# Kernel optimization log

Measured on AMD Instinct MI355X. Metric: run time of the kernel, lower is better.

The kernel has to match this reference:

```python
import jax, jax.numpy as jnp
import numpy as np
from jax import lax


def _l2n(t, eps=1e-12):
    n = jnp.sqrt(jnp.sum(t * t, axis=-1, keepdims=True))
    return t / jnp.maximum(n, eps)


def _ln(t, w, b, eps=1e-5):
    mu = jnp.mean(t, -1, keepdims=True)
    var = jnp.var(t, -1, keepdims=True)
    return (t - mu) / jnp.sqrt(var + eps) * w + b


def _unfold3(x):
    # nn.Unfold(kernel_size=3, padding=1, stride=1): [B,C,H,W] -> [B,C,9,H*W]
    B, C, H, W = x.shape
    xp = jnp.pad(x, ((0, 0), (0, 0), (1, 1), (1, 1)))
    pat = jnp.stack([xp[:, :, i:i + H, j:j + W] for i in range(3) for j in range(3)], axis=2)
    return pat.reshape(B, C, 9, H * W)


def _forward(x, norm1_w, norm1_b, q_w, q_b, kv_w, kv_b, temperature, query_embedding,
             learnable_tokens, learnable_bias, sr_w, sr_b, pln_w, pln_b, proj_w, proj_b,
             norm2_w, norm2_b, fc1_w, fc1_b, dw_w, dw_b, fc2_w, fc2_b):
    B, C, H, W = x.shape
    nh = temperature.shape[0]
    d = C // nh
    N = H * W
    K = 9  # local_len = window_size**2
    # norm1 (WithBias LayerNorm over channel dim, channels-last)
    y = _ln(x.reshape(B, C, N).transpose(0, 2, 1), norm1_w, norm1_b)  # [B,N,C]
    # ---- AggregatedAttention ----
    q = (y @ q_w.T + q_b).reshape(B, N, nh, d).transpose(0, 2, 1, 3)  # [B,h,N,d]
    qn = _l2n(q)
    qs = (qn + query_embedding) * jax.nn.softplus(temperature)
    kv = y @ kv_w.T + kv_b  # [B,N,2C]
    k_loc = _l2n(kv[..., :C].reshape(B, N, nh, d)).reshape(B, N, C)
    kvl = jnp.concatenate([k_loc, kv[..., C:]], -1).transpose(0, 2, 1).reshape(B, 2 * C, H, W)
    pat = _unfold3(kvl).reshape(B, 2 * nh, d, K, N).transpose(0, 1, 4, 2, 3)  # [B,2h,N,d,K]
    k_l, v_l = pat[:, :nh], pat[:, nh:]
    attn_local = jnp.einsum('bhnd,bhndk->bhnk', qs, k_l)  # [B,h,N,K]
    # pooled branch; sr_ratio=1 so adaptive_avg_pool2d is identity
    y4 = y.transpose(0, 2, 1).reshape(B, C, H, W)
    xp = jax.nn.gelu(jnp.einsum('oc,bchw->bohw', sr_w, y4) + sr_b[:, None, None], approximate=False)
    xp = _ln(xp.reshape(B, C, N).transpose(0, 2, 1), pln_w, pln_b)  # [B,pool_len,C]
    kvp = (xp @ kv_w.T + kv_b).reshape(B, N, 2 * nh, d).transpose(0, 2, 1, 3)
    k_p = _l2n(kvp[:, :nh])
    v_p = kvp[:, nh:]
    attn_pool = jnp.einsum('bhnd,bhmd->bhnm', qs, k_p)  # [B,h,N,pool_len]
    attn = jax.nn.softmax(jnp.concatenate([attn_local, attn_pool], -1), axis=-1)
    a_l, a_p = attn[..., :K], attn[..., K:]
    w_l = jnp.einsum('bhnd,hdk->bhnk', qn, learnable_tokens) + learnable_bias + a_l
    x_local = jnp.einsum('bhnk,bhndk->bhnd', w_l, v_l)
    x_pool = jnp.einsum('bhnm,bhmd->bhnd', a_p, v_p)
    xo = (x_local + x_pool).transpose(0, 2, 1, 3).reshape(B, N, C)
    # proj then raw torch-style reshape [B,N,C] -> [B,C,H,W] (memory reinterpretation)
    xo = (xo @ proj_w.T + proj_b).reshape(B, C, H, W)
    x = x + xo
    # ---- ConvolutionalGLU MLP ----
    hf = dw_b.shape[0]
    y2 = _ln(x.reshape(B, C, N).transpose(0, 2, 1), norm2_w, norm2_b).transpose(0, 2, 1).reshape(B, C, H, W)
    f1 = jnp.einsum('oc,bchw->bohw', fc1_w, y2) + fc1_b[:, None, None]
    a, v = f1[:, :hf], f1[:, hf:]
    dw = lax.conv_general_dilated(a, dw_w, (1, 1), ((1, 1), (1, 1)),
                                  feature_group_count=hf,
                                  dimension_numbers=('NCHW', 'OIHW', 'NCHW')) + dw_b[:, None, None]
    g = jax.nn.gelu(dw, approximate=False) * v
    out = jnp.einsum('oc,bchw->bohw', fc2_w, g) + fc2_b[:, None, None]
    return x + out


def setup_inputs() -> dict:
    key = jax.random.key(0)
    B, C, H, W = 2, 128, 56, 56
    nh, d, K = 4, 32, 9
    hf = int(2 * int(C * 4.0) / 3)  # 341
    ks = iter(jax.random.split(key, 16))
    rn = lambda shape, s=0.02: jax.random.normal(next(ks), shape, jnp.float32) * s
    return {
        'x': jax.random.normal(next(ks), (B, C, H, W), jnp.float32),
        'norm1_w': jnp.ones((C,), jnp.float32), 'norm1_b': jnp.zeros((C,), jnp.float32),
        'q_w': rn((C, C)), 'q_b': jnp.zeros((C,), jnp.float32),
        'kv_w': rn((2 * C, C)), 'kv_b': jnp.zeros((2 * C,), jnp.float32),
        'temperature': jnp.full((nh, 1, 1), float(np.log(np.exp(1.0 / 0.24) - 1.0)), jnp.float32),
        'query_embedding': rn((nh, 1, d)),
        'learnable_tokens': rn((nh, d, K)),
        'learnable_bias': jnp.zeros((nh, 1, K), jnp.float32),
        'sr_w': rn((C, C)), 'sr_b': jnp.zeros((C,), jnp.float32),
        'pln_w': jnp.ones((C,), jnp.float32), 'pln_b': jnp.zeros((C,), jnp.float32),
        'proj_w': rn((C, C)), 'proj_b': jnp.zeros((C,), jnp.float32),
        'norm2_w': jnp.ones((C,), jnp.float32), 'norm2_b': jnp.zeros((C,), jnp.float32),
        'fc1_w': rn((2 * hf, C)), 'fc1_b': jnp.zeros((2 * hf,), jnp.float32),
        'dw_w': rn((hf, 1, 3, 3)), 'dw_b': jnp.zeros((hf,), jnp.float32),
        'fc2_w': rn((C, hf)), 'fc2_b': jnp.zeros((C,), jnp.float32),
    }


def reference(x, norm1_w, norm1_b, q_w, q_b, kv_w, kv_b, temperature, query_embedding,
              learnable_tokens, learnable_bias, sr_w, sr_b, pln_w, pln_b, proj_w, proj_b,
              norm2_w, norm2_b, fc1_w, fc1_b, dw_w, dw_b, fc2_w, fc2_b):
    return _forward(x, norm1_w, norm1_b, q_w, q_b, kv_w, kv_b, temperature, query_embedding,
                    learnable_tokens, learnable_bias, sr_w, sr_b, pln_w, pln_b, proj_w, proj_b,
                    norm2_w, norm2_b, fc1_w, fc1_b, dw_w, dw_b, fc2_w, fc2_b)
```

## Files before the change

### kernel.cpp

```cpp
#include <hip/hip_runtime.h>
#include <hip/hip_bf16.h>

typedef __hip_bfloat16 bf16;
typedef short s8v __attribute__((ext_vector_type(8)));
typedef short s4v __attribute__((ext_vector_type(4)));
typedef float f4v __attribute__((ext_vector_type(4)));

#define DEVI __device__ __forceinline__

DEVI float cvt(float x){ return x; }
DEVI float cvt(bf16 x){ return __bfloat162float(x); }

DEVI void stg(float* p, float v){ *p = v; }
DEVI void stg(bf16* p, float v){ *p = __float2bfloat16(v); }

DEVI float gelu_exact(float x){
  return 0.5f*x*(1.0f + erff(x*0.70710678118654752440f));
}

constexpr int B_ = 2, C_ = 128, H_ = 56, W_ = 56, N_ = 3136, NH_ = 4, D_ = 32, HF_ = 341;
constexpr int ROWS_ = B_*N_;
constexpr int KF2 = 352;
constexpr int GQ_ = NH_*B_*N_;
constexpr int FW = 512;
constexpr int KSP = 12;
constexpr int SPLIT = 256;
constexpr float LOG2E = 1.4426950408889634f;
constexpr float E8L2  = 11.541560327111707f;

template<typename TX, typename TY, bool PLANES>
__global__ __launch_bounds__(256)
void ln_kernel(const TX* __restrict__ x, long xstr, const float* __restrict__ w,
               const float* __restrict__ bia, TY* __restrict__ y)
{
  int gid = blockIdx.x*4 + (threadIdx.x>>6);
  int lane = threadIdx.x & 63;
  int b = gid / N_, n = gid % N_;
  float v0, v1;
  if (PLANES){
    v0 = cvt(x[((long)b*C_ + lane     )*N_ + n]);
    v1 = cvt(x[((long)b*C_ + lane + 64)*N_ + n]);
  } else {
    v0 = cvt(x[(long)gid*xstr + lane     ]);
    v1 = cvt(x[(long)gid*xstr + lane + 64]);
  }
  float s = v0+v1, ss = v0*v0 + v1*v1;
  #pragma unroll
  for (int o=32;o>0;o>>=1){ s += __shfl_xor(s,o); ss += __shfl_xor(ss,o); }
  float mu  = s*(1.0f/128.0f);
  float var = fmaxf(ss*(1.0f/128.0f) - mu*mu, 0.f);
  float inv = rsqrtf(var + 1e-5f);
  stg(&y[(long)gid*C_ + lane     ], (v0-mu)*inv*w[lane     ] + bia[lane     ]);
  stg(&y[(long)gid*C_ + lane + 64], (v1-mu)*inv*w[lane + 64] + bia[lane + 64]);
}

__global__ __launch_bounds__(256)
void head_kernel(const float* __restrict__ q_w, const float* __restrict__ kv_w,
                 const float* __restrict__ sr_w, const float* __restrict__ proj_w,
                 const float* __restrict__ fc1_w, const float* __restrict__ fc2_w,
                 const float* __restrict__ q_b, const float* __restrict__ kv_b,
                 const float* __restrict__ sr_b,
                 bf16* __restrict__ out, float* __restrict__ bias_out,
                 const float* __restrict__ x_in, const float* __restrict__ n1w,
                 const float* __restrict__ n1b, bf16* __restrict__ y)
{
  if (blockIdx.x >= 839){
    int gid = (blockIdx.x - 839)*4 + (threadIdx.x>>6);
    int lane = threadIdx.x & 63;
    int b = gid / N_, n = gid % N_;
    float v0 = x_in[((long)b*C_ + lane     )*N_ + n];
    float v1 = x_in[((long)b*C_ + lane + 64)*N_ + n];
    float s = v0+v1, ss = v0*v0 + v1*v1;
    #pragma unroll
    for (int o=32;o>0;o>>=1){ s += __shfl_xor(s,o); ss += __shfl_xor(ss,o); }
    float mu  = s*(1.0f/128.0f);
    float var = fmaxf(ss*(1.0f/128.0f) - mu*mu, 0.f);
    float inv = rsqrtf(var + 1e-5f);
    y[(long)gid*C_ + lane     ] = __float2bfloat16((v0-mu)*inv*n1w[lane     ] + n1b[lane     ]);
    y[(long)gid*C_ + lane + 64] = __float2bfloat16((v1-mu)*inv*n1w[lane + 64] + n1b[lane + 64]);
    return;
  }
  int t = blockIdx.x*256 + threadIdx.x;
  if (t >= 214272){
    int i = t - 214272;
    if (i < 512){
      float bv = (i < 128) ? q_b[i] : (i < 384) ? kv_b[i-128] : sr_b[i-384];
      bias_out[i] = bv;
    }
    return;
  }
  float v;
  if      (t <  16384) v = q_w[t];
  else if (t <  49152) v = kv_w[t-16384];
  else if (t <  65536) v = sr_w[t-49152];
  else if (t <  81920) v = proj_w[t-65536];
  else if (t < 169216) v = fc1_w[t-81920];
  else {
    int i = t - 169216; int m = i / KF2, kp = i % KF2;
    v = (kp < HF_) ? fc2_w[m*HF_ + kp] : 0.f;
  }
  out[t] = __float2bfloat16(v);
}

template<int KT, int MODE, typename TC, int BM=64, int LDA=KT, int NCH=1>
__global__ __launch_bounds__(256)
void gemm_mfma(const bf16* __restrict__ A, const bf16* __restrict__ B,
               const float* __restrict__ bias, const float* __restrict__ res,
               TC* __restrict__ Cm, int M, int Nn,
               long sA, long sB, long sC, long sR,
               const float* __restrict__ qe, const float* __restrict__ temp,
               bf16* __restrict__ aux0, bf16* __restrict__ aux1)
{
  A  += (long)blockIdx.z * sA;
  B  += (long)blockIdx.z * sB;
  Cm += (long)blockIdx.z * sC;
  if (res) res += (long)blockIdx.z * sR;
  int lane = threadIdx.x & 63, w = threadIdx.x >> 6;
  int m = lane & 15, quad = lane >> 4;
  int n0 = blockIdx.x*64, m0 = blockIdx.y*BM;
  const bf16* ap[NCH];
  #pragma unroll
  for (int cc=0; cc<NCH; cc++){
    int ar = m0 + cc*64 + w*16 + m;
    if (ar >= M) ar = M-1;
    ap[cc] = A + (long)ar*LDA + quad*8;
  }
  const bf16* bp = B + (long)(n0 + m)*KT + quad*8;
  s8v a4[KT/32];
  if (MODE==7){
    float s=0.f, ssum=0.f;
    #pragma unroll
    for (int i=0;i<KT/32;i++){
      a4[i] = *(const s8v*)(ap[0] + i*32);
      #pragma unroll
      for (int j=0;j<8;j++){
        float v = cvt(((const bf16*)&a4[i])[j]);
        s += v; ssum = fmaf(v,v,ssum);
      }
    }
    s    += __shfl_xor(s,16);    s    += __shfl_xor(s,32);
    ssum += __shfl_xor(ssum,16); ssum += __shfl_xor(ssum,32);
    float mu  = s*(1.0f/128.0f);
    float var = fmaxf(ssum*(1.0f/128.0f) - mu*mu, 0.f);
    float inv = rsqrtf(var + 1e-5f);
    #pragma unroll
    for (int i=0;i<KT/32;i++){
      #pragma unroll
      for (int j=0;j<8;j++){
        int c = i*32 + quad*8 + j;
        float v = cvt(((const bf16*)&a4[i])[j]);
        ((bf16*)&a4[i])[j] = __float2bfloat16((v-mu)*inv*qe[c] + temp[c]);
      }
    }
  }
  f4v acc[NCH][4];
  #pragma unroll
  for (int cc=0; cc<NCH; cc++)
    #pragma unroll
    for (int s=0;s<4;s++) acc[cc][s] = (f4v){0.f,0.f,0.f,0.f};
  #pragma unroll
  for (int k0 = 0; k0 < KT; k0 += 32){
    s8v bf[4];
    #pragma unroll
    for (int s=0;s<4;s++) bf[s] = *(const s8v*)(bp + (long)s*16*KT + k0);
    #pragma unroll
    for (int cc=0; cc<NCH; cc++){
      s8v af = (MODE==7) ? a4[k0/32] : *(const s8v*)(ap[cc] + k0);
      #pragma unroll
      for (int s=0;s<4;s++)
        acc[cc][s] = __builtin_amdgcn_mfma_f32_16x16x32_bf16(af, bf[s], acc[cc][s], 0, 0, 0);
    }
  }
  if ((MODE==6 || MODE==7) && blockIdx.x < 2){
    int hA = blockIdx.x*2, hB = hA+1;
    float spA = 0.f, spB = 0.f;
    if (MODE==6){
      spA = log1pf(expf(temp[hA])) * LOG2E;
      spB = log1pf(expf(temp[hB])) * LOG2E;
    }
    #pragma unroll
    for (int cc=0; cc<NCH; cc++){
      #pragma unroll
      for (int r=0;r<4;r++){
        float v4[4];
        #pragma unroll
        for (int s=0;s<4;s++) v4[s] = acc[cc][s][r] + bias[n0 + s*16 + m];
        float ssA = v4[0]*v4[0] + v4[1]*v4[1];
        float ssB = v4[2]*v4[2] + v4[3]*v4[3];
        #pragma unroll
        for (int off=1; off<16; off<<=1){
          ssA += __shfl_xor(ssA, off);
          ssB += __shfl_xor(ssB, off);
        }
        float invA = 1.f/fmaxf(sqrtf(ssA), 1e-12f);
        float invB = 1.f/fmaxf(sqrtf(ssB), 1e-12f);
        int gm = m0 + cc*64 + w*16 + quad*4 + r;
        int b = gm / N_, n = gm % N_;
        #pragma unroll
        for (int s=0;s<4;s++){
          int h = (s<2) ? hA : hB;
          int d = (s&1)*16 + m;
          float v = v4[s] * ((s<2) ? invA : invB);
          if (MODE==6) v = (v + qe[h*D_ + d]) * ((s<2) ? spA : spB);
          aux0[((long)(b*NH_+h)*N_ + n)*D_ + d] = __float2bfloat16(v);
        }
      }
    }
    return;
  }
  if (MODE==7){
    int gm0 = m0 + w*16 + quad*4;
    int b = gm0 / N_, nb = gm0 % N_;
    #pragma unroll
    for (int s=0;s<4;s++){
      int h = (blockIdx.x-2)*2 + (s>>1);
      int d = (s&1)*16 + m;
      bf16 p4[4];
      #pragma unroll
      for (int r=0;r<4;r++) p4[r] = __float2bfloat16(acc[0][s][r] + bias[n0 + s*16 + m]);
      *(s4v*)(aux1 + ((long)(b*NH_+h)*D_ + d)*N_ + nb) = *(const s4v*)p4;
    }
    return;
  }
  #pragma unroll
  for (int cc=0; cc<NCH; cc++){
    int m0c = m0 + cc*64;
    #pragma unroll
    for (int s=0;s<4;s++){
      int gn = n0 + s*16 + m;
      #pragma unroll
      for (int r=0;r<4;r++){
        int gm = m0c + w*16 + quad*4 + r;
        if (gm >= M) continue;
        float v = acc[cc][s][r];
        if (MODE==1 || MODE==4 || MODE==6) v += bias[gn];
        else                               v += bias[gm];
        if (MODE==6 && gn >= 384) v = gelu_exact(v);
        if (MODE==4 || MODE==5) v += res[(long)gm*Nn + gn];
        stg(&Cm[(long)gm*Nn + gn], v);
      }
    }
  }
}

__global__ __launch_bounds__(256)
void attn_part_kernel(const bf16* __restrict__ qs_, const bf16* __restrict__ kp_,
                      const bf16* __restrict__ vp_,
                      bf16* __restrict__ Op, float* __restrict__ Lp)
{
  int bh = blockIdx.y;
  int z  = blockIdx.z;
  int lane = threadIdx.x & 63;
  int w    = threadIdx.x >> 6;
  int m    = lane & 15, quad = lane >> 4;
  int base = blockIdx.x*256 + w*16;

  s8v af[4]; bool hasQ[4];
  #pragma unroll
  for (int ch=0; ch<4; ch++){
    int qq = base + ch*64;
    hasQ[ch] = (qq < N_);
    af[ch] = *(const s8v*)(qs_ + ((long)bh*N_ + (hasQ[ch] ? qq : base) + m)*D_ + quad*8);
  }
  const bf16* kpb = kp_ + (long)bh*N_*D_;
  const bf16* vpb = vp_ + (long)bh*D_*N_;
  int kperm = (m & 3) + 8*(m >> 2);
  f4v o0[4], o1[4];
  float l[4];
  #pragma unroll
  for (int ch=0; ch<4; ch++){
    o0[ch] = (f4v){0.f,0.f,0.f,0.f}; o1[ch] = (f4v){0.f,0.f,0.f,0.f};
    l[ch] = 0.f;
  }

  auto loadKV = [&](s8v* kf, s8v* vf, int t){
    kf[0] = *(const s8v*)(kpb + (long)(t + kperm     )*D_ + quad*8);
    kf[1] = *(const s8v*)(kpb + (long)(t + kperm +  4)*D_ + quad*8);
    kf[2] = *(const s8v*)(kpb + (long)(t + kperm + 32)*D_ + quad*8);
    kf[3] = *(const s8v*)(kpb + (long)(t + kperm + 36)*D_ + quad*8);
    vf[0] = *(const s8v*)(vpb + (long)(m     )*N_ + t      + quad*8);
    vf[1] = *(const s8v*)(vpb + (long)(16 + m)*N_ + t      + quad*8);
    vf[2] = *(const s8v*)(vpb + (long)(m     )*N_ + t + 32 + quad*8);
    vf[3] = *(const s8v*)(vpb + (long)(16 + m)*N_ + t + 32 + quad*8);
  };
  auto compute = [&](const s8v* kf, const s8v* vf){
    __builtin_amdgcn_s_setprio(1);
    #pragma unroll
    for (int ch=0; ch<4; ch++){
      f4v c[4];
      #pragma unroll
      for (int s=0;s<4;s++){
        c[s] = (f4v){-E8L2, -E8L2, -E8L2, -E8L2};
        c[s] = __builtin_amdgcn_mfma_f32_16x16x32_bf16(kf[s], af[ch], c[s], 0, 0, 0);
      }
      bf16 p8a[8], p8b[8];
      float ls = 0.f;
      #pragma unroll
      for (int r=0;r<4;r++){
        float ea = __builtin_amdgcn_exp2f(c[0][r]);
        float eb = __builtin_amdgcn_exp2f(c[1][r]);
        float ec = __builtin_amdgcn_exp2f(c[2][r]);
        float ed = __builtin_amdgcn_exp2f(c[3][r]);
        ls += (ea+eb) + (ec+ed);
        p8a[r] = __float2bfloat16(ea); p8a[4+r] = __float2bfloat16(eb);
        p8b[r] = __float2bfloat16(ec); p8b[4+r] = __float2bfloat16(ed);
      }
      l[ch] += ls;
      s8v pa = *(const s8v*)p8a, pb = *(const s8v*)p8b;
      o0[ch] = __builtin_amdgcn_mfma_f32_16x16x32_bf16(pa, vf[0], o0[ch], 0, 0, 0);
      o1[ch] = __builtin_amdgcn_mfma_f32_16x16x32_bf16(pa, vf[1], o1[ch], 0, 0, 0);
      o0[ch] = __builtin_amdgcn_mfma_f32_16x16x32_bf16(pb, vf[2], o0[ch], 0, 0, 0);
      o1[ch] = __builtin_amdgcn_mfma_f32_16x16x32_bf16(pb, vf[3], o1[ch], 0, 0, 0);
    }
    __builtin_amdgcn_s_setprio(0);
  };

  int tlo = z*SPLIT, thi = (z==KSP-1) ? N_ : tlo + SPLIT;
  s8v kfA[4], vfA[4], kfB[4], vfB[4];
  int t0 = tlo;
  loadKV(kfA, vfA, t0);
  for (;;){
    if (t0 + 64 < thi) loadKV(kfB, vfB, t0 + 64);
    compute(kfA, vfA);
    t0 += 64;
    if (t0 >= thi) break;
    if (t0 + 64 < thi) loadKV(kfA, vfA, t0 + 64);
    compute(kfB, vfB);
    t0 += 64;
    if (t0 >= thi) break;
  }
  #pragma unroll
  for (int ch=0; ch<4; ch++){
    if (!hasQ[ch]) continue;
    float lr = l[ch];
    lr += __shfl_xor(lr, 16);
    lr += __shfl_xor(lr, 32);
    long gqBase = (long)bh*N_ + base + ch*64;
    #pragma unroll
    for (int r=0;r<4;r++){
      bf16* op = Op + ((long)z*GQ_ + gqBase + quad*4 + r)*32;
      op[m]      = __float2bfloat16(o0[ch][r]);
      op[16 + m] = __float2bfloat16(o1[ch][r]);
    }
    if (quad == 0) Lp[(long)z*GQ_ + gqBase + m] = lr;
  }
}

__global__ __launch_bounds__(256)
void attn_combine_kernel(const bf16* __restrict__ Op, const float* __restrict__ Lp,
                         const bf16* __restrict__ qs_, const bf16* __restrict__ fused,
                         const float* __restrict__ qe, const float* __restrict__ temp,
                         const float* __restrict__ tokens, const float* __restrict__ tbias,
                         bf16* __restrict__ xo)
{
  int t  = blockIdx.x*256 + threadIdx.x;
  int gq = t >> 3;
  int l8 = t & 7;
  int d0 = l8*4;
  int n = gq % N_; int bh = gq / N_; int h = bh & 3; int b = bh >> 2;
  float out[4] = {0.f,0.f,0.f,0.f};
  #pragma unroll
  for (int z=0; z<KSP; z++){
    s4v o4 = *(const s4v*)(Op + ((long)z*GQ_ + gq)*32 + d0);
    #pragma unroll
    for (int j=0;j<4;j++) out[j] += cvt(((const bf16*)&o4)[j]);
  }
  float L = 0.f;
  for (int z=l8; z<KSP; z+=8) L += Lp[(long)z*GQ_ + gq];
  #pragma unroll
  for (int off=1; off<8; off<<=1) L += __shfl_xor(L, off);
  float q[4];
  {
    s4v q4 = *(const s4v*)(qs_ + (long)gq*D_ + d0);
    #pragma unroll
    for (int j=0;j<4;j++) q[j] = cvt(((const bf16*)&q4)[j]) * 0.6931471805599453f;
  }
  int hy = n / W_, wx = n % W_;
  const bf16* kvb = fused + (long)b*N_*FW + 128 + h*D_ + d0;
  float sl[9];
  #pragma unroll
  for (int k=0;k<9;k++){
    int di = k/3-1, dj = k%3-1;
    int yy = hy+di, xx = wx+dj;
    bool ok = (yy>=0 && yy<H_ && xx>=0 && xx<W_);
    float dot = 0.f, ss = 0.f;
    if (ok){
      s4v k4 = *(const s4v*)(kvb + (long)(yy*W_+xx)*FW);
      #pragma unroll
      for (int j=0;j<4;j++){
        float kk = cvt(((const bf16*)&k4)[j]);
        dot = fmaf(q[j], kk, dot);
        ss  = fmaf(kk, kk, ss);
      }
    }
    #pragma unroll
    for (int off=1; off<8; off<<=1){
      dot += __shfl_xor(dot, off);
      ss  += __shfl_xor(ss,  off);
    }
    sl[k] = ok ? dot / fmaxf(sqrtf(ss), 1e-12f) : 0.f;
  }
  #pragma unroll
  for (int k=0;k<9;k++) L += __expf(sl[k] - 8.f);
  float invL = 1.f/L;
  #pragma unroll
  for (int j=0;j<4;j++) out[j] *= invL;
  float sp = log1pf(expf(temp[h]));
  float invsp = 1.f/sp;
  float qn[4];
  #pragma unroll
  for (int j=0;j<4;j++) qn[j] = q[j]*invsp - qe[h*D_ + d0 + j];
  #pragma unroll
  for (int k=0;k<9;k++){
    float tok = 0.f;
    #pragma unroll
    for (int j=0;j<4;j++) tok = fmaf(qn[j], tokens[(h*D_ + d0 + j)*9 + k], tok);
    #pragma unroll
    for (int off=1; off<8; off<<=1) tok += __shfl_xor(tok, off);
    float wl = tok + tbias[h*9+k] + __expf(sl[k] - 8.f)*invL;
    int di = k/3-1, dj = k%3-1;
    int yy = hy+di, xx = wx+dj;
    if (yy>=0 && yy<H_ && xx>=0 && xx<W_){
      s4v v4 = *(const s4v*)(kvb + (long)(yy*W_+xx)*FW + 128);
      #pragma unroll
      for (int j=0;j<4;j++) out[j] = fmaf(wl, cvt(((const bf16*)&v4)[j]), out[j]);
    }
  }
  bf16 o4[4];
  #pragma unroll
  for (int j=0;j<4;j++) o4[j] = __float2bfloat16(out[j]);
  *(s4v*)(xo + ((long)(b*N_ + n))*C_ + h*D_ + d0) = *(const s4v*)o4;
}

__global__ __launch_bounds__(256)
void dwconv_kernel(const bf16* __restrict__ f1, const float* __restrict__ dww,
                   const float* __restrict__ dwb, bf16* __restrict__ g)
{
  int t = blockIdx.x*256 + threadIdx.x;
  if (t >= B_*N_*44) return;
  int b = t / (N_*44); int r = t - b*(N_*44);
  int n = r % N_, cg = r / N_;
  f1 += (long)b*2*HF_*N_;
  g  += (long)b*N_*KF2;
  int c0 = cg*8;
  int hy = n / W_, wx = n % W_;
  bf16 o8[8];
  #pragma unroll
  for (int j=0;j<8;j++){
    int c = c0 + j;
    float val = 0.f;
    if (c < HF_){
      const bf16* ap = f1 + (long)c*N_;
      float s = dwb[c];
      #pragma unroll
      for (int di=-1; di<=1; di++)
        #pragma unroll
        for (int dj=-1; dj<=1; dj++){
          int yy = hy+di, xx = wx+dj;
          if (yy>=0 && yy<H_ && xx>=0 && xx<W_)
            s = fmaf(dww[c*9 + (di+1)*3 + (dj+1)], cvt(ap[yy*W_+xx]), s);
        }
      val = gelu_exact(s) * cvt(f1[(long)(HF_+c)*N_ + n]);
    }
    o8[j] = __float2bfloat16(val);
  }
  *(s8v*)(g + (long)n*KF2 + c0) = *(const s8v*)o8;
}

extern "C" void kernel_launch(void* const* d_in, const int* in_sizes, int n_in,
                              void* d_out, int out_size, void* d_ws, size_t ws_size,
                              hipStream_t stream)
{
  (void)in_sizes; (void)n_in; (void)out_size; (void)ws_size;
  const float* x_in      = (const float*)d_in[0];
  const float* norm1_w   = (const float*)d_in[1];
  const float* norm1_b   = (const float*)d_in[2];
  const float* q_w       = (const float*)d_in[3];
  const float* q_b       = (const float*)d_in[4];
  const float* kv_w      = (const float*)d_in[5];
  const float* kv_b      = (const float*)d_in[6];
  const float* temp      = (const float*)d_in[7];
  const float* qe        = (const float*)d_in[8];
  const float* tokens    = (const float*)d_in[9];
  const float* tbias     = (const float*)d_in[10];
  const float* sr_w      = (const float*)d_in[11];
  const float* sr_b      = (const float*)d_in[12];
  const float* pln_w     = (const float*)d_in[13];
  const float* pln_b     = (const float*)d_in[14];
  const float* proj_w    = (const float*)d_in[15];
  const float* proj_b    = (const float*)d_in[16];
  const float* norm2_w   = (const float*)d_in[17];
  const float* norm2_b   = (const float*)d_in[18];
  const float* fc1_w     = (const float*)d_in[19];
  const float* fc1_b     = (const float*)d_in[20];
  const float* dw_w      = (const float*)d_in[21];
  const float* dw_b      = (const float*)d_in[22];
  const float* fc2_w     = (const float*)d_in[23];
  const float* fc2_b     = (const float*)d_in[24];

  char* w8 = (char*)d_ws;
  bf16*  fused   = (bf16*)(w8 + 0);
  float* x2      = (float*)(w8 + 0);
  bf16*  y2      = (bf16*)(w8 + 3211264);
  bf16*  f1b     = (bf16*)(w8 + 4816896);
  bf16*  qs      = (bf16*)(w8 + 6422528);
  bf16*  k_p     = (bf16*)(w8 + 9633792);
  bf16*  v_p     = (bf16*)(w8 + 11239424);
  bf16*  Opart   = (bf16*)(w8 + 13045056);
  bf16*  g_rows  = (bf16*)(w8 + 32312640);
  bf16*  wbase   = (bf16*)(w8 + 36728128);
  float* fbias   = (float*)(w8 + 37156672);
  bf16*  y       = f1b;
  bf16*  xo      = (bf16*)d_out;
  float* Lpart   = (float*)((char*)d_out + 1605632);
  bf16*  proj_wb = wbase + 65536;
  bf16*  fc1_wb  = wbase + 81920;
  bf16*  fc2_wb  = wbase + 169216;

  head_kernel<<<839 + ROWS_/4, 256, 0, stream>>>(
      q_w, kv_w, sr_w, proj_w, fc1_w, fc2_w, q_b, kv_b, sr_b, wbase, fbias,
      x_in, norm1_w, norm1_b, y);
  gemm_mfma<128, 6, bf16, 128, 128, 2><<<dim3(8,49), 256, 0, stream>>>(
      y, wbase, fbias, nullptr, fused, ROWS_, FW, 0,0,0,0, qe, temp, qs, nullptr);
  gemm_mfma<128, 7, bf16, 64, FW><<<dim3(4,98), 256, 0, stream>>>(
      fused + 384, wbase + 16384, kv_b, nullptr, (bf16*)nullptr, ROWS_, 256, 0,0,0,0,
      pln_w, pln_b, k_p, v_p);
  attn_part_kernel<<<dim3(13,8,KSP), 256, 0, stream>>>(qs, k_p, v_p, Opart, Lpart);
  attn_combine_kernel<<<GQ_*8/256, 256, 0, stream>>>(Opart, Lpart, qs, fused,
                                                     qe, temp, tokens, tbias, xo);
  gemm_mfma<128, 4, float, 16><<<dim3(2,392), 64, 0, stream>>>(
      xo, proj_wb, proj_b, x_in, x2, ROWS_, 128, 0,0,0,0, nullptr, nullptr, nullptr, nullptr);
  ln_kernel<float, bf16, true><<<ROWS_/4, 256, 0, stream>>>(x2, 0, norm2_w, norm2_b, y2);
  gemm_mfma<128, 3, bf16, 128, 128, 2><<<dim3(49,6,B_), 256, 0, stream>>>(
      fc1_wb, y2, fc1_b, nullptr, f1b, 2*HF_, N_,
      0, (long)N_*C_, (long)2*HF_*N_, 0, nullptr, nullptr, nullptr, nullptr);
  dwconv_kernel<<<(B_*N_*44+255)/256, 256, 0, stream>>>(f1b, dw_w, dw_b, g_rows);
  gemm_mfma<KF2, 5, float, 16><<<dim3(49,8,B_), 64, 0, stream>>>(
      fc2_wb, g_rows, fc2_b, x2, (float*)d_out, C_, N_,
      0, (long)N_*KF2, (long)C_*N_, (long)C_*N_, nullptr, nullptr, nullptr, nullptr);
}
```

Measured before the change: 240.2 us.

## Tile LayerNorm transposes through shared memory and row-vectorize depthwise conv

The channel-planar LayerNorms (norm1 inside head_kernel and norm2) now load 16-token by 128-channel tiles with coalesced vector reads into padded shared memory, reduce per token, and write bf16 rows with 8-wide stores. Before, each access was strided across channel planes. The depthwise conv kernel now gives each thread one channel and eight consecutive pixels, reusing a sliding window of vector-loaded inputs instead of reloading up to 9 neighbours per output. In exchange, the conv writes its output one element at a time with a KF2 stride per pixel, so its stores are no longer coalesced.

```diff
diff --git a/kernel.cpp b/kernel.cpp
--- a/kernel.cpp
+++ b/kernel.cpp
@@ -25,33 +25,68 @@
 constexpr int FW = 512;
 constexpr int KSP = 12;
 constexpr int SPLIT = 256;
+constexpr int NTILE = 392;
 constexpr float LOG2E = 1.4426950408889634f;
 constexpr float E8L2  = 11.541560327111707f;
 
-template<typename TX, typename TY, bool PLANES>
+DEVI void ln_tile_body(int tile, int t, const float* __restrict__ x,
+                       const float* __restrict__ w, const float* __restrict__ bia,
+                       bf16* __restrict__ y, float* sm , float* st )
+{
+  int b = tile / 196, nb = (tile % 196) * 16;
+  {
+    int c = t >> 1, half = t & 1;
+    const float* xp = x + ((long)b*C_ + c)*N_ + nb + half*8;
+    f4v v0 = *(const f4v*)xp;
+    f4v v1 = *(const f4v*)(xp + 4);
+    #pragma unroll
+    for (int j=0;j<4;j++){
+      sm[c*17 + half*8 + j    ] = v0[j];
+      sm[c*17 + half*8 + 4 + j] = v1[j];
+    }
+  }
+  __syncthreads();
+  {
+    int i = t >> 4, k = t & 15;
+    float s = 0.f, ss = 0.f;
+    #pragma unroll
+    for (int u=0;u<8;u++){
+      float v = sm[(k + u*16)*17 + i];
+      s += v; ss = fmaf(v,v,ss);
+    }
+    #pragma unroll
+    for (int off=1; off<16; off<<=1){
+      s  += __shfl_xor(s,  off);
+      ss += __shfl_xor(ss, off);
+    }
+    if (k == 0){
+      float mu  = s*(1.0f/128.0f);
+      float var = fmaxf(ss*(1.0f/128.0f) - mu*mu, 0.f);
+      st[i]      = mu;
+      st[16 + i] = rsqrtf(var + 1e-5f);
+    }
+  }
+  __syncthreads();
+  {
+    int i = t >> 4, c0 = (t & 15)*8;
+    float mu = st[i], inv = st[16 + i];
+    bf16 o8[8];
+    #pragma unroll
+    for (int j=0;j<8;j++){
+      int c = c0 + j;
+      o8[j] = __float2bfloat16((sm[c*17 + i] - mu)*inv*w[c] + bia[c]);
+    }
+    *(s8v*)(y + ((long)(b*N_ + nb + i))*C_ + c0) = *(const s8v*)o8;
+  }
+}
+
 __global__ __launch_bounds__(256)
-void ln_kernel(const TX* __restrict__ x, long xstr, const float* __restrict__ w,
-               const float* __restrict__ bia, TY* __restrict__ y)
-{
-  int gid = blockIdx.x*4 + (threadIdx.x>>6);
-  int lane = threadIdx.x & 63;
-  int b = gid / N_, n = gid % N_;
-  float v0, v1;
-  if (PLANES){
-    v0 = cvt(x[((long)b*C_ + lane     )*N_ + n]);
-    v1 = cvt(x[((long)b*C_ + lane + 64)*N_ + n]);
-  } else {
-    v0 = cvt(x[(long)gid*xstr + lane     ]);
-    v1 = cvt(x[(long)gid*xstr + lane + 64]);
-  }
-  float s = v0+v1, ss = v0*v0 + v1*v1;
-  #pragma unroll
-  for (int o=32;o>0;o>>=1){ s += __shfl_xor(s,o); ss += __shfl_xor(ss,o); }
-  float mu  = s*(1.0f/128.0f);
-  float var = fmaxf(ss*(1.0f/128.0f) - mu*mu, 0.f);
-  float inv = rsqrtf(var + 1e-5f);
-  stg(&y[(long)gid*C_ + lane     ], (v0-mu)*inv*w[lane     ] + bia[lane     ]);
-  stg(&y[(long)gid*C_ + lane + 64], (v1-mu)*inv*w[lane + 64] + bia[lane + 64]);
+void ln_tile_kernel(const float* __restrict__ x, const float* __restrict__ w,
+                    const float* __restrict__ bia, bf16* __restrict__ y)
+{
+  __shared__ float sm[128*17];
+  __shared__ float st[32];
+  ln_tile_body(blockIdx.x, threadIdx.x, x, w, bia, y, sm, st);
 }
 
 __global__ __launch_bounds__(256)
@@ -64,20 +99,10 @@
                  const float* __restrict__ x_in, const float* __restrict__ n1w,
                  const float* __restrict__ n1b, bf16* __restrict__ y)
 {
+  __shared__ float sm[128*17];
+  __shared__ float st[32];
   if (blockIdx.x >= 839){
-    int gid = (blockIdx.x - 839)*4 + (threadIdx.x>>6);
-    int lane = threadIdx.x & 63;
-    int b = gid / N_, n = gid % N_;
-    float v0 = x_in[((long)b*C_ + lane     )*N_ + n];
-    float v1 = x_in[((long)b*C_ + lane + 64)*N_ + n];
-    float s = v0+v1, ss = v0*v0 + v1*v1;
-    #pragma unroll
-    for (int o=32;o>0;o>>=1){ s += __shfl_xor(s,o); ss += __shfl_xor(ss,o); }
-    float mu  = s*(1.0f/128.0f);
-    float var = fmaxf(ss*(1.0f/128.0f) - mu*mu, 0.f);
-    float inv = rsqrtf(var + 1e-5f);
-    y[(long)gid*C_ + lane     ] = __float2bfloat16((v0-mu)*inv*n1w[lane     ] + n1b[lane     ]);
-    y[(long)gid*C_ + lane + 64] = __float2bfloat16((v1-mu)*inv*n1w[lane + 64] + n1b[lane + 64]);
+    ln_tile_body(blockIdx.x - 839, threadIdx.x, x_in, n1w, n1b, y, sm, st);
     return;
   }
   int t = blockIdx.x*256 + threadIdx.x;
@@ -437,34 +462,44 @@
                    const float* __restrict__ dwb, bf16* __restrict__ g)
 {
   int t = blockIdx.x*256 + threadIdx.x;
-  if (t >= B_*N_*44) return;
-  int b = t / (N_*44); int r = t - b*(N_*44);
-  int n = r % N_, cg = r / N_;
+  int b = t / (352*392); int r = t - b*(352*392);
+  int c = r / 392, chunk = r - c*392;
+  int y = chunk / 7, x0 = (chunk - y*7)*8;
   f1 += (long)b*2*HF_*N_;
-  g  += (long)b*N_*KF2;
-  int c0 = cg*8;
-  int hy = n / W_, wx = n % W_;
-  bf16 o8[8];
+  bf16* gb = g + (long)b*N_*KF2 + c;
+  if (c >= HF_){
+    #pragma unroll
+    for (int j=0;j<8;j++) gb[(long)(y*W_ + x0 + j)*KF2] = __float2bfloat16(0.f);
+    return;
+  }
+  const bf16* ap = f1 + (long)c*N_;
+  float acc[8];
+  #pragma unroll
+  for (int j=0;j<8;j++) acc[j] = dwb[c];
+  #pragma unroll
+  for (int dy=-1; dy<=1; dy++){
+    int yy = y + dy;
+    if (yy < 0 || yy >= H_) continue;
+    int base = yy*W_ + x0;
+    s8v mid = *(const s8v*)(ap + base);
+    float wnd[10];
+    wnd[0] = (x0 > 0)      ? cvt(ap[base-1]) : 0.f;
+    #pragma unroll
+    for (int j=0;j<8;j++) wnd[1+j] = cvt(((const bf16*)&mid)[j]);
+    wnd[9] = (x0 + 8 < W_) ? cvt(ap[base+8]) : 0.f;
+    float k0 = dww[c*9 + (dy+1)*3    ];
+    float k1 = dww[c*9 + (dy+1)*3 + 1];
+    float k2 = dww[c*9 + (dy+1)*3 + 2];
+    #pragma unroll
+    for (int j=0;j<8;j++)
+      acc[j] = fmaf(k0, wnd[j], fmaf(k1, wnd[j+1], fmaf(k2, wnd[j+2], acc[j])));
+  }
+  s8v g8 = *(const s8v*)(f1 + (long)(HF_+c)*N_ + y*W_ + x0);
   #pragma unroll
   for (int j=0;j<8;j++){
-    int c = c0 + j;
-    float val = 0.f;
-    if (c < HF_){
-      const bf16* ap = f1 + (long)c*N_;
-      float s = dwb[c];
-      #pragma unroll
-      for (int di=-1; di<=1; di++)
-        #pragma unroll
-        for (int dj=-1; dj<=1; dj++){
-          int yy = hy+di, xx = wx+dj;
-          if (yy>=0 && yy<H_ && xx>=0 && xx<W_)
-            s = fmaf(dww[c*9 + (di+1)*3 + (dj+1)], cvt(ap[yy*W_+xx]), s);
-        }
-      val = gelu_exact(s) * cvt(f1[(long)(HF_+c)*N_ + n]);
-    }
-    o8[j] = __float2bfloat16(val);
-  }
-  *(s8v*)(g + (long)n*KF2 + c0) = *(const s8v*)o8;
+    float val = gelu_exact(acc[j]) * cvt(((const bf16*)&g8)[j]);
+    gb[(long)(y*W_ + x0 + j)*KF2] = __float2bfloat16(val);
+  }
 }
 
 extern "C" void kernel_launch(void* const* d_in, const int* in_sizes, int n_in,
@@ -517,7 +552,7 @@
   bf16*  fc1_wb  = wbase + 81920;
   bf16*  fc2_wb  = wbase + 169216;
 
-  head_kernel<<<839 + ROWS_/4, 256, 0, stream>>>(
+  head_kernel<<<839 + NTILE, 256, 0, stream>>>(
       q_w, kv_w, sr_w, proj_w, fc1_w, fc2_w, q_b, kv_b, sr_b, wbase, fbias,
       x_in, norm1_w, norm1_b, y);
   gemm_mfma<128, 6, bf16, 128, 128, 2><<<dim3(8,49), 256, 0, stream>>>(
@@ -530,11 +565,11 @@
                                                      qe, temp, tokens, tbias, xo);
   gemm_mfma<128, 4, float, 16><<<dim3(2,392), 64, 0, stream>>>(
       xo, proj_wb, proj_b, x_in, x2, ROWS_, 128, 0,0,0,0, nullptr, nullptr, nullptr, nullptr);
-  ln_kernel<float, bf16, true><<<ROWS_/4, 256, 0, stream>>>(x2, 0, norm2_w, norm2_b, y2);
+  ln_tile_kernel<<<NTILE, 256, 0, stream>>>(x2, norm2_w, norm2_b, y2);
   gemm_mfma<128, 3, bf16, 128, 128, 2><<<dim3(49,6,B_), 256, 0, stream>>>(
       fc1_wb, y2, fc1_b, nullptr, f1b, 2*HF_, N_,
       0, (long)N_*C_, (long)2*HF_*N_, 0, nullptr, nullptr, nullptr, nullptr);
-  dwconv_kernel<<<(B_*N_*44+255)/256, 256, 0, stream>>>(f1b, dw_w, dw_b, g_rows);
+  dwconv_kernel<<<(B_*352*392)/256, 256, 0, stream>>>(f1b, dw_w, dw_b, g_rows);
   gemm_mfma<KF2, 5, float, 16><<<dim3(49,8,B_), 64, 0, stream>>>(
       fc2_wb, g_rows, fc2_b, x2, (float*)d_out, C_, N_,
       0, (long)N_*KF2, (long)C_*N_, (long)C_*N_, nullptr, nullptr, nullptr, nullptr);
```

Measured after the change: 229.7 us. 4.4% less time.
